# Kernel tuning notes

Hardware: AMD Instinct MI355X
Metric: run time of the kernel (lower is better)

Reference implementation:

```python
import jax, jax.numpy as jnp
import numpy as np

WEIGHTS = (0.5, 1.0, 2.0)   # per-channel weights (init kwarg)
INVERTED = True             # init kwarg


def setup_inputs() -> dict:
    key = jax.random.key(0)
    B, C, H, W = 16, 3, 256, 256
    # binary flood mask: nonzero = foreground (scipy EDT measures distance to nearest zero)
    flood = jax.random.randint(key, (B, C, H, W), 0, 2).astype(jnp.float32)
    return {"flood_batch": flood}


def _edt_squared(mask):
    """Exact squared Euclidean distance transform per [H,W] slice.

    mask: bool [B,C,H,W], True = foreground (nonzero). Returns float32 [B,C,H,W]
    squared distance from each True pixel to the nearest False pixel (0 at False).
    Uses the exact separable decomposition:
      D2[r,w] = min_{r'} ( g[r',w]^2 + (r-r')^2 ),  g = 1D horizontal distance to zero.
    """
    B, C, H, W = mask.shape
    BIG = jnp.float32(H + W)  # exceeds any achievable 1D distance

    # --- pass 1: 1D distance to nearest zero along W (forward + backward scans) ---
    m = jnp.moveaxis(mask, -1, 0)  # [W,B,C,H]

    def step(carry, mm):
        d = jnp.where(mm, jnp.minimum(carry + 1.0, BIG), 0.0)
        return d, d

    init = jnp.full((B, C, H), BIG, jnp.float32)
    _, fwd = jax.lax.scan(step, init, m)
    _, bwd = jax.lax.scan(step, init, m[::-1])
    g = jnp.minimum(fwd, bwd[::-1])          # [W,B,C,H]
    g2 = jnp.moveaxis(g, 0, -1) ** 2          # [B,C,H,W]

    # --- pass 2: exact min-plus over rows (vectorized over B,C,W; scan over output row) ---
    rows = jnp.arange(H, dtype=jnp.float32)

    def row_step(_, r):
        cand = g2 + ((r - rows) ** 2)[None, None, :, None]  # [B,C,H,W]
        return None, cand.min(axis=2)                        # [B,C,W]

    _, d2 = jax.lax.scan(row_step, None, rows)  # [H,B,C,W]
    return jnp.moveaxis(d2, 0, 2)               # [B,C,H,W]


def reference(flood_batch):
    w = jnp.asarray(WEIGHTS, jnp.float32)
    dt = jnp.sqrt(_edt_squared(flood_batch != 0))            # [B,C,H,W]
    dt = dt * w[None, :, None, None]                         # per-channel weight
    mx = dt.max(axis=(2, 3), keepdims=True)                  # per-slice max
    safe = jnp.where(mx > 0, mx, 1.0)
    scaled = (mx - dt) / safe if INVERTED else dt / safe
    return jnp.where(mx > 0, scaled, dt)
```

## Files before the change

kernel.cpp:

```cpp
#include <hip/hip_runtime.h>


#define PADV 1e30f

__global__ __launch_bounds__(256) void k1_g16(const float* __restrict__ in,
                                              unsigned short* __restrict__ g) {
    int row = blockIdx.x * 4 + (threadIdx.x >> 6);
    int lane = threadIdx.x & 63;
    const float4 m = ((const float4*)in)[(long)row * 64 + lane];

    unsigned long long b[4];
    b[0] = __ballot(m.x == 0.f);
    b[1] = __ballot(m.y == 0.f);
    b[2] = __ballot(m.z == 0.f);
    b[3] = __ballot(m.w == 0.f);

    unsigned long long loP = ~0ull >> (63 - lane);
    unsigned long long loM = loP >> 1;
    unsigned long long hiP = ~0ull << lane;
    unsigned long long hiM = hiP << 1;

    int LP[4], LM[4], RP[4], RM[4];
    #pragma unroll
    for (int cc = 0; cc < 4; ++cc) {
        unsigned long long mlp = b[cc] & loP;
        unsigned long long mlm = b[cc] & loM;
        unsigned long long mhp = b[cc] & hiP;
        unsigned long long mhm = b[cc] & hiM;
        LP[cc] = mlp ? 4 * (63 - __builtin_clzll(mlp)) + cc : -1000;
        LM[cc] = mlm ? 4 * (63 - __builtin_clzll(mlm)) + cc : -1000;
        RP[cc] = mhp ? 4 * __builtin_ctzll(mhp) + cc : 2000;
        RM[cc] = mhm ? 4 * __builtin_ctzll(mhm) + cc : 2000;
    }
    int qp1 = max(LP[0], LP[1]);
    int qp2 = max(qp1, LP[2]);
    int qp3 = max(qp2, LP[3]);
    int sm3 = LM[3];
    int sm2 = max(LM[2], sm3);
    int sm1 = max(LM[1], sm2);
    int colL0 = max(LP[0], sm1);
    int colL1 = max(qp1, sm2);
    int colL2 = max(qp2, sm3);
    int colL3 = qp3;
    int sp2 = min(RP[2], RP[3]);
    int sp1 = min(RP[1], sp2);
    int sp0 = min(RP[0], sp1);
    int pm0 = RM[0];
    int pm1 = min(pm0, RM[1]);
    int pm2 = min(pm1, RM[2]);
    int colR0 = sp0;
    int colR1 = min(pm0, sp1);
    int colR2 = min(pm1, sp2);
    int colR3 = min(pm2, RP[3]);

    int p0 = lane * 4;
    int d0 = min(min(p0 - colL0, colR0 - p0), 512);
    int d1 = min(min(p0 + 1 - colL1, colR1 - p0 - 1), 512);
    int d2 = min(min(p0 + 2 - colL2, colR2 - p0 - 2), 512);
    int d3 = min(min(p0 + 3 - colL3, colR3 - p0 - 3), 512);

    ushort4 v;
    v.x = (unsigned short)d0; v.y = (unsigned short)d1;
    v.z = (unsigned short)d2; v.w = (unsigned short)d3;
    ((ushort4*)(g + (long)row * 256))[lane] = v;
}

__global__ __launch_bounds__(256) __attribute__((amdgpu_waves_per_eu(4)))
void k2_colpass(const unsigned short* __restrict__ g,
                float* __restrict__ d2out,
                float* __restrict__ stripmax) {
    __shared__ float tile[16 * 101];
    __shared__ float wm[4];
    int bx = blockIdx.x;
    int slice = bx >> 6;
    int sub = bx & 63;
    int strip = sub >> 2;
    int quarter = sub & 3;
    int w0 = strip * 16;
    int base = quarter * 64;
    int tid = threadIdx.x;

    if (tid < 192) {
        int idx = tid >> 1;
        int half = tid & 1;
        int colbase = half * 8;
        int r = base - 16 + idx;
        if (r >= 0 && r < 256) {
            uint4 q = *(const uint4*)(g + (long)slice * 65536 + (long)r * 256 + w0 + colbase);
            unsigned vv[4] = {q.x, q.y, q.z, q.w};
            #pragma unroll
            for (int e = 0; e < 4; ++e) {
                float dl = (float)(vv[e] & 0xffffu);
                float dh = (float)(vv[e] >> 16);
                tile[(colbase + 2 * e) * 101 + idx] = dl * dl;
                tile[(colbase + 2 * e + 1) * 101 + idx] = dh * dh;
            }
        } else {
            #pragma unroll
            for (int e = 0; e < 8; ++e) tile[(colbase + e) * 101 + idx] = PADV;
        }
    }
    __syncthreads();

    int c = tid & 15;
    int rg = tid >> 4;
    int i0 = 16 + rg * 4;

    float own[4], lo[16], hi[16];
    #pragma unroll
    for (int k = 0; k < 4; ++k) own[k] = tile[c * 101 + i0 + k];
    #pragma unroll
    for (int i = 0; i < 16; ++i) {
        lo[i] = tile[c * 101 + i0 - 16 + i];
        hi[i] = tile[c * 101 + i0 + 4 + i];
    }

    float dmin[4];
    #pragma unroll
    for (int k = 0; k < 4; ++k) dmin[k] = own[k];
    #pragma unroll
    for (int o = 1; o <= 16; ++o) {
        float oo = (float)(o * o);
        #pragma unroll
        for (int k = 0; k < 4; ++k) {
            int jm = k - o, jp = k + o;
            float a = (jm >= 0) ? own[jm] : lo[jm + 16];
            float b = (jp < 4) ? own[jp] : hi[jp - 4];
            dmin[k] = fminf(dmin[k], fminf(a, b) + oo);
        }
    }

    int p = w0 + c;
    int r0 = base + rg * 4;
    #pragma unroll
    for (int k = 0; k < 4; ++k) {
        if (dmin[k] > 288.0f) {
            float best = dmin[k];
            int r = r0 + k;
            const unsigned short* col = g + (long)slice * 65536 + p;
            for (int rp = 0; rp < 256; ++rp) {
                float gv = (float)col[rp * 256];
                float dr = (float)(r - rp);
                best = fminf(best, fmaf(dr, dr, gv * gv));
            }
            dmin[k] = best;
        }
    }

    float* dst = d2out + (long)slice * 65536 + w0 + c;
    float mmax = 0.f;
    #pragma unroll
    for (int k = 0; k < 4; ++k) {
        dst[(long)(r0 + k) * 256] = dmin[k];
        mmax = fmaxf(mmax, dmin[k]);
    }
    #pragma unroll
    for (int off = 32; off >= 1; off >>= 1)
        mmax = fmaxf(mmax, __shfl_down(mmax, off, 64));
    if ((tid & 63) == 0) wm[tid >> 6] = mmax;
    __syncthreads();
    if (tid == 0)
        stripmax[bx] = fmaxf(fmaxf(wm[0], wm[1]), fmaxf(wm[2], wm[3]));
}

__global__ __launch_bounds__(256) void k3_final(float* __restrict__ out,
                                                const float* __restrict__ stripmax) {
    __shared__ float sMx;
    int tid = threadIdx.x;
    int slice = blockIdx.x >> 5;
    if (tid < 64) {
        float v = stripmax[slice * 64 + tid];
        #pragma unroll
        for (int off = 32; off >= 1; off >>= 1) v = fmaxf(v, __shfl_down(v, off, 64));
        if (tid == 0) sMx = v;
    }
    __syncthreads();

    int ch = slice % 3;
    float wgt = (ch == 0) ? 0.5f : ((ch == 1) ? 1.0f : 2.0f);
    float mx = wgt * __builtin_sqrtf(sMx);

    int idx4 = blockIdx.x * 512 + tid;
    float4* o4 = (float4*)out;
    #pragma unroll
    for (int rep = 0; rep < 2; ++rep) {
        int i4 = idx4 + rep * 256;
        float4 d2 = o4[i4];
        float4 r;
        if (mx > 0.f) {
            float inv = 1.0f / mx;
            r.x = (mx - wgt * __builtin_sqrtf(d2.x)) * inv;
            r.y = (mx - wgt * __builtin_sqrtf(d2.y)) * inv;
            r.z = (mx - wgt * __builtin_sqrtf(d2.z)) * inv;
            r.w = (mx - wgt * __builtin_sqrtf(d2.w)) * inv;
        } else {
            r.x = wgt * __builtin_sqrtf(d2.x);
            r.y = wgt * __builtin_sqrtf(d2.y);
            r.z = wgt * __builtin_sqrtf(d2.z);
            r.w = wgt * __builtin_sqrtf(d2.w);
        }
        o4[i4] = r;
    }
}

extern "C" void kernel_launch(void* const* d_in, const int* in_sizes, int n_in,
                              void* d_out, int out_size, void* d_ws, size_t ws_size,
                              hipStream_t stream) {
    const float* in = (const float*)d_in[0];
    float* out = (float*)d_out;
    float* stripmax = (float*)d_ws;
    unsigned short* g = (unsigned short*)((char*)d_ws + 16384);

    k1_g16<<<3072, 256, 0, stream>>>(in, g);
    k2_colpass<<<3072, 256, 0, stream>>>(g, out, stripmax);
    k3_final<<<1536, 256, 0, stream>>>(out, stripmax);
}
```

Baseline: 81.73 us.

## Fuse row-distance pass into column pass with full-width 16-row slabs in LDS

Merges the horizontal 1D distance kernel into the vertical min-plus kernel, so each block recomputes the row distances for a 48-row halo window of full-width rows directly into shared memory. This removes the uint16 intermediate buffer round-trip and one launch. Each thread now owns one column and 16 output rows, which uses more registers and cuts the grid to 768 blocks. The rare fallback for distances beyond the halo now brute-forces the whole slice from the input mask instead of scanning a precomputed column, which is far more expensive if it ever triggers.

```diff
diff --git a/kernel.cpp b/kernel.cpp
--- a/kernel.cpp
+++ b/kernel.cpp
@@ -3,175 +3,154 @@
 
 #define PADV 1e30f
 
-__global__ __launch_bounds__(256) void k1_g16(const float* __restrict__ in,
-                                              unsigned short* __restrict__ g) {
-    int row = blockIdx.x * 4 + (threadIdx.x >> 6);
-    int lane = threadIdx.x & 63;
-    const float4 m = ((const float4*)in)[(long)row * 64 + lane];
-
-    unsigned long long b[4];
-    b[0] = __ballot(m.x == 0.f);
-    b[1] = __ballot(m.y == 0.f);
-    b[2] = __ballot(m.z == 0.f);
-    b[3] = __ballot(m.w == 0.f);
-
-    unsigned long long loP = ~0ull >> (63 - lane);
-    unsigned long long loM = loP >> 1;
-    unsigned long long hiP = ~0ull << lane;
-    unsigned long long hiM = hiP << 1;
-
-    int LP[4], LM[4], RP[4], RM[4];
-    #pragma unroll
-    for (int cc = 0; cc < 4; ++cc) {
-        unsigned long long mlp = b[cc] & loP;
-        unsigned long long mlm = b[cc] & loM;
-        unsigned long long mhp = b[cc] & hiP;
-        unsigned long long mhm = b[cc] & hiM;
-        LP[cc] = mlp ? 4 * (63 - __builtin_clzll(mlp)) + cc : -1000;
-        LM[cc] = mlm ? 4 * (63 - __builtin_clzll(mlm)) + cc : -1000;
-        RP[cc] = mhp ? 4 * __builtin_ctzll(mhp) + cc : 2000;
-        RM[cc] = mhm ? 4 * __builtin_ctzll(mhm) + cc : 2000;
-    }
-    int qp1 = max(LP[0], LP[1]);
-    int qp2 = max(qp1, LP[2]);
-    int qp3 = max(qp2, LP[3]);
-    int sm3 = LM[3];
-    int sm2 = max(LM[2], sm3);
-    int sm1 = max(LM[1], sm2);
-    int colL0 = max(LP[0], sm1);
-    int colL1 = max(qp1, sm2);
-    int colL2 = max(qp2, sm3);
-    int colL3 = qp3;
-    int sp2 = min(RP[2], RP[3]);
-    int sp1 = min(RP[1], sp2);
-    int sp0 = min(RP[0], sp1);
-    int pm0 = RM[0];
-    int pm1 = min(pm0, RM[1]);
-    int pm2 = min(pm1, RM[2]);
-    int colR0 = sp0;
-    int colR1 = min(pm0, sp1);
-    int colR2 = min(pm1, sp2);
-    int colR3 = min(pm2, RP[3]);
-
-    int p0 = lane * 4;
-    int d0 = min(min(p0 - colL0, colR0 - p0), 512);
-    int d1 = min(min(p0 + 1 - colL1, colR1 - p0 - 1), 512);
-    int d2 = min(min(p0 + 2 - colL2, colR2 - p0 - 2), 512);
-    int d3 = min(min(p0 + 3 - colL3, colR3 - p0 - 3), 512);
-
-    ushort4 v;
-    v.x = (unsigned short)d0; v.y = (unsigned short)d1;
-    v.z = (unsigned short)d2; v.w = (unsigned short)d3;
-    ((ushort4*)(g + (long)row * 256))[lane] = v;
-}
-
-__global__ __launch_bounds__(256) __attribute__((amdgpu_waves_per_eu(4)))
-void k2_colpass(const unsigned short* __restrict__ g,
-                float* __restrict__ d2out,
-                float* __restrict__ stripmax) {
-    __shared__ float tile[16 * 101];
+__global__ __launch_bounds__(256) __attribute__((amdgpu_waves_per_eu(3)))
+void kfused(const float* __restrict__ in,
+            float* __restrict__ d2out,
+            float* __restrict__ slabmax) {
+    __shared__ __align__(16) float tile[48 * 260];
     __shared__ float wm[4];
     int bx = blockIdx.x;
-    int slice = bx >> 6;
-    int sub = bx & 63;
-    int strip = sub >> 2;
-    int quarter = sub & 3;
-    int w0 = strip * 16;
-    int base = quarter * 64;
+    int slice = bx >> 4;
+    int slab = bx & 15;
+    int r0 = slab * 16;
     int tid = threadIdx.x;
+    int lane = tid & 63;
+    int wv = tid >> 6;
 
-    if (tid < 192) {
-        int idx = tid >> 1;
-        int half = tid & 1;
-        int colbase = half * 8;
-        int r = base - 16 + idx;
-        if (r >= 0 && r < 256) {
-            uint4 q = *(const uint4*)(g + (long)slice * 65536 + (long)r * 256 + w0 + colbase);
-            unsigned vv[4] = {q.x, q.y, q.z, q.w};
-            #pragma unroll
-            for (int e = 0; e < 4; ++e) {
-                float dl = (float)(vv[e] & 0xffffu);
-                float dh = (float)(vv[e] >> 16);
-                tile[(colbase + 2 * e) * 101 + idx] = dl * dl;
-                tile[(colbase + 2 * e + 1) * 101 + idx] = dh * dh;
+    {
+        unsigned long long loP = ~0ull >> (63 - lane);
+        unsigned long long loM = loP >> 1;
+        unsigned long long hiP = ~0ull << lane;
+        unsigned long long hiM = hiP << 1;
+        #pragma unroll
+        for (int i = 0; i < 12; ++i) {
+            int ti = wv * 12 + i;
+            int r = r0 - 16 + ti;
+            float4 res;
+            if (r >= 0 && r < 256) {
+                const float4 m = ((const float4*)(in + (long)slice * 65536 + (long)r * 256))[lane];
+                unsigned long long b[4];
+                b[0] = __ballot(m.x == 0.f);
+                b[1] = __ballot(m.y == 0.f);
+                b[2] = __ballot(m.z == 0.f);
+                b[3] = __ballot(m.w == 0.f);
+
+                int LP[4], LM[4], RP[4], RM[4];
+                #pragma unroll
+                for (int cc = 0; cc < 4; ++cc) {
+                    unsigned long long mlp = b[cc] & loP;
+                    unsigned long long mlm = b[cc] & loM;
+                    unsigned long long mhp = b[cc] & hiP;
+                    unsigned long long mhm = b[cc] & hiM;
+                    LP[cc] = mlp ? 4 * (63 - __builtin_clzll(mlp)) + cc : -1000;
+                    LM[cc] = mlm ? 4 * (63 - __builtin_clzll(mlm)) + cc : -1000;
+                    RP[cc] = mhp ? 4 * __builtin_ctzll(mhp) + cc : 2000;
+                    RM[cc] = mhm ? 4 * __builtin_ctzll(mhm) + cc : 2000;
+                }
+                int qp1 = max(LP[0], LP[1]);
+                int qp2 = max(qp1, LP[2]);
+                int qp3 = max(qp2, LP[3]);
+                int sm3 = LM[3];
+                int sm2 = max(LM[2], sm3);
+                int sm1 = max(LM[1], sm2);
+                int colL0 = max(LP[0], sm1);
+                int colL1 = max(qp1, sm2);
+                int colL2 = max(qp2, sm3);
+                int colL3 = qp3;
+                int sp2 = min(RP[2], RP[3]);
+                int sp1 = min(RP[1], sp2);
+                int sp0 = min(RP[0], sp1);
+                int pm0 = RM[0];
+                int pm1 = min(pm0, RM[1]);
+                int pm2 = min(pm1, RM[2]);
+                int colR0 = sp0;
+                int colR1 = min(pm0, sp1);
+                int colR2 = min(pm1, sp2);
+                int colR3 = min(pm2, RP[3]);
+
+                int p0 = lane * 4;
+                int d0 = min(min(p0 - colL0, colR0 - p0), 512);
+                int d1 = min(min(p0 + 1 - colL1, colR1 - p0 - 1), 512);
+                int d2 = min(min(p0 + 2 - colL2, colR2 - p0 - 2), 512);
+                int d3 = min(min(p0 + 3 - colL3, colR3 - p0 - 3), 512);
+                float f0 = (float)d0, f1 = (float)d1, f2 = (float)d2, f3 = (float)d3;
+                res.x = f0 * f0; res.y = f1 * f1; res.z = f2 * f2; res.w = f3 * f3;
+            } else {
+                res.x = PADV; res.y = PADV; res.z = PADV; res.w = PADV;
             }
-        } else {
-            #pragma unroll
-            for (int e = 0; e < 8; ++e) tile[(colbase + e) * 101 + idx] = PADV;
+            ((float4*)(tile + ti * 260))[lane] = res;
         }
     }
     __syncthreads();
 
-    int c = tid & 15;
-    int rg = tid >> 4;
-    int i0 = 16 + rg * 4;
-
-    float own[4], lo[16], hi[16];
-    #pragma unroll
-    for (int k = 0; k < 4; ++k) own[k] = tile[c * 101 + i0 + k];
+    int c = tid;
+    float lo[16], own[16], hi[16];
     #pragma unroll
     for (int i = 0; i < 16; ++i) {
-        lo[i] = tile[c * 101 + i0 - 16 + i];
-        hi[i] = tile[c * 101 + i0 + 4 + i];
+        lo[i] = tile[i * 260 + c];
+        own[i] = tile[(16 + i) * 260 + c];
+        hi[i] = tile[(32 + i) * 260 + c];
     }
 
-    float dmin[4];
+    float dmin[16];
     #pragma unroll
-    for (int k = 0; k < 4; ++k) dmin[k] = own[k];
+    for (int k = 0; k < 16; ++k) dmin[k] = own[k];
     #pragma unroll
     for (int o = 1; o <= 16; ++o) {
         float oo = (float)(o * o);
         #pragma unroll
-        for (int k = 0; k < 4; ++k) {
+        for (int k = 0; k < 16; ++k) {
             int jm = k - o, jp = k + o;
             float a = (jm >= 0) ? own[jm] : lo[jm + 16];
-            float b = (jp < 4) ? own[jp] : hi[jp - 4];
+            float b = (jp < 16) ? own[jp] : hi[jp - 16];
             dmin[k] = fminf(dmin[k], fminf(a, b) + oo);
         }
     }
 
-    int p = w0 + c;
-    int r0 = base + rg * 4;
     #pragma unroll
-    for (int k = 0; k < 4; ++k) {
+    for (int k = 0; k < 16; ++k) {
         if (dmin[k] > 288.0f) {
             float best = dmin[k];
             int r = r0 + k;
-            const unsigned short* col = g + (long)slice * 65536 + p;
+            const float* sl = in + (long)slice * 65536;
             for (int rp = 0; rp < 256; ++rp) {
-                float gv = (float)col[rp * 256];
-                float dr = (float)(r - rp);
-                best = fminf(best, fmaf(dr, dr, gv * gv));
+                float dr2 = (float)((r - rp) * (r - rp));
+                for (int cp = 0; cp < 256; ++cp) {
+                    if (sl[rp * 256 + cp] == 0.f) {
+                        float dc = (float)(c - cp);
+                        best = fminf(best, fmaf(dc, dc, dr2));
+                    }
+                }
             }
             dmin[k] = best;
         }
     }
 
-    float* dst = d2out + (long)slice * 65536 + w0 + c;
+    float* dst = d2out + (long)slice * 65536 + c;
     float mmax = 0.f;
     #pragma unroll
-    for (int k = 0; k < 4; ++k) {
+    for (int k = 0; k < 16; ++k) {
         dst[(long)(r0 + k) * 256] = dmin[k];
         mmax = fmaxf(mmax, dmin[k]);
     }
     #pragma unroll
     for (int off = 32; off >= 1; off >>= 1)
         mmax = fmaxf(mmax, __shfl_down(mmax, off, 64));
-    if ((tid & 63) == 0) wm[tid >> 6] = mmax;
+    if (lane == 0) wm[wv] = mmax;
     __syncthreads();
     if (tid == 0)
-        stripmax[bx] = fmaxf(fmaxf(wm[0], wm[1]), fmaxf(wm[2], wm[3]));
+        slabmax[bx] = fmaxf(fmaxf(wm[0], wm[1]), fmaxf(wm[2], wm[3]));
 }
 
 __global__ __launch_bounds__(256) void k3_final(float* __restrict__ out,
-                                                const float* __restrict__ stripmax) {
+                                                const float* __restrict__ slabmax) {
     __shared__ float sMx;
     int tid = threadIdx.x;
     int slice = blockIdx.x >> 5;
-    if (tid < 64) {
-        float v = stripmax[slice * 64 + tid];
+    if (tid < 16) {
+        float v = slabmax[slice * 16 + tid];
         #pragma unroll
-        for (int off = 32; off >= 1; off >>= 1) v = fmaxf(v, __shfl_down(v, off, 64));
+        for (int off = 8; off >= 1; off >>= 1) v = fmaxf(v, __shfl_down(v, off, 64));
         if (tid == 0) sMx = v;
     }
     __syncthreads();
@@ -208,10 +187,8 @@
                               hipStream_t stream) {
     const float* in = (const float*)d_in[0];
     float* out = (float*)d_out;
-    float* stripmax = (float*)d_ws;
-    unsigned short* g = (unsigned short*)((char*)d_ws + 16384);
+    float* slabmax = (float*)d_ws;
 
-    k1_g16<<<3072, 256, 0, stream>>>(in, g);
-    k2_colpass<<<3072, 256, 0, stream>>>(g, out, stripmax);
-    k3_final<<<1536, 256, 0, stream>>>(out, stripmax);
+    kfused<<<768, 256, 0, stream>>>(in, out, slabmax);
+    k3_final<<<1536, 256, 0, stream>>>(out, slabmax);
 }
```

New measurement: 86.06 us. +5.3%, slower.
